# Kernel optimization log

Measured on AMD Instinct MI355X. Metric: run time of the kernel, lower is better.

## Reference

```python
import jax, jax.numpy as jnp
import numpy as np

E = 200_000   # edges (messages)
T = 2_000_000 # triplets
N = 20_000    # atoms/nodes
H = 128       # hidden_channels
INT = 64      # int_emb_size
BAS = 8       # basis_emb_size
OUT_EMB = 256 # out_emb_channels
NRAD = 6
SBF_DIM = 7 * 6  # num_spherical * num_radial = 42
NB = 4        # num_blocks
OUTC = 1      # num_targets


def setup_inputs() -> dict:
    key = jax.random.key(0)
    ks = iter(jax.random.split(key, 64))

    def w(shape):
        # glorot-ish scaled weights, stored as [in, out] for x @ W
        return jax.random.normal(next(ks), shape, jnp.float32) / np.sqrt(shape[-2])

    return dict(
        x=jax.random.normal(next(ks), (E, H), jnp.float32),
        rbf=jax.random.normal(next(ks), (E, NRAD), jnp.float32),
        sbf=jax.random.normal(next(ks), (T, SBF_DIM), jnp.float32),
        # interaction block params, stacked over NB blocks
        W_rbf1=w((NB, NRAD, BAS)), W_rbf2=w((NB, BAS, H)),
        W_sbf1=w((NB, SBF_DIM, BAS)), W_sbf2=w((NB, BAS, INT)),
        W_kj=w((NB, H, H)), b_kj=jnp.zeros((NB, H), jnp.float32),
        W_ji=w((NB, H, H)), b_ji=jnp.zeros((NB, H), jnp.float32),
        W_down=w((NB, H, INT)), W_up=w((NB, INT, H)),
        Wb=w((NB, 2, H, H)), bb=jnp.zeros((NB, 2, H), jnp.float32),   # num_before_skip=1 -> 2 linears
        Wa=w((NB, 4, H, H)), ba=jnp.zeros((NB, 4, H), jnp.float32),   # num_after_skip=2 -> 4 linears
        W_lin=w((NB, H, H)), b_lin=jnp.zeros((NB, H), jnp.float32),
        # output block params, stacked over NB+1 blocks
        Wo_rbf=w((NB + 1, NRAD, H)),
        Wo_up=w((NB + 1, H, OUT_EMB)), bo_up=jnp.zeros((NB + 1, OUT_EMB), jnp.float32),
        Wo_lins=w((NB + 1, 3, OUT_EMB, OUT_EMB)), bo_lins=jnp.zeros((NB + 1, 3, OUT_EMB), jnp.float32),
        Wo_out=w((NB + 1, OUT_EMB, OUTC)),
        idx_kj=jax.random.randint(next(ks), (T,), 0, E, jnp.int32),
        idx_ji=jax.random.randint(next(ks), (T,), 0, E, jnp.int32),
        idx_i=jax.random.randint(next(ks), (E,), 0, N, jnp.int32),
        num_nodes=N,
    )


def _interaction(b, x, rbf, sbf, idx_kj, idx_ji, p):
    act = jax.nn.silu
    x_ji = act(x @ p['W_ji'][b] + p['b_ji'][b])
    x_kj = act(x @ p['W_kj'][b] + p['b_kj'][b])
    rbf_t = (rbf @ p['W_rbf1'][b]) @ p['W_rbf2'][b]          # [E,H]
    x_kj = act((x_kj * rbf_t) @ p['W_down'][b])              # [E,INT]
    sbf_t = (sbf @ p['W_sbf1'][b]) @ p['W_sbf2'][b]          # [T,INT]
    m = x_kj[idx_kj] * sbf_t                                  # triplet gather [T,INT]
    agg = jax.ops.segment_sum(m, idx_ji, num_segments=x.shape[0])  # scatter-add [E,INT]
    x_kj = act(agg @ p['W_up'][b])                            # [E,H]
    h = x_ji + x_kj
    # residual layers before skip (1 layer = 2 linears)
    h = h + act(act(h @ p['Wb'][b, 0] + p['bb'][b, 0]) @ p['Wb'][b, 1] + p['bb'][b, 1])
    h = act(h @ p['W_lin'][b] + p['b_lin'][b]) + x
    # residual layers after skip (2 layers = 4 linears)
    for l in range(2):
        h = h + act(act(h @ p['Wa'][b, 2 * l] + p['ba'][b, 2 * l]) @ p['Wa'][b, 2 * l + 1] + p['ba'][b, 2 * l + 1])
    return h


def _output(b, x, rbf, idx_i, num_nodes, p):
    act = jax.nn.silu
    t = (rbf @ p['Wo_rbf'][b]) * x                            # [E,H]
    t = jax.ops.segment_sum(t, idx_i, num_segments=num_nodes) # [N,H]
    t = t @ p['Wo_up'][b] + p['bo_up'][b]
    for l in range(3):
        t = act(t @ p['Wo_lins'][b, l] + p['bo_lins'][b, l])
    return t @ p['Wo_out'][b]                                 # [N,OUTC]


def reference(x, rbf, sbf, W_rbf1, W_rbf2, W_sbf1, W_sbf2, W_kj, b_kj, W_ji, b_ji,
              W_down, W_up, Wb, bb, Wa, ba, W_lin, b_lin,
              Wo_rbf, Wo_up, bo_up, Wo_lins, bo_lins, Wo_out,
              idx_kj, idx_ji, idx_i, num_nodes):
    p = dict(W_rbf1=W_rbf1, W_rbf2=W_rbf2, W_sbf1=W_sbf1, W_sbf2=W_sbf2,
             W_kj=W_kj, b_kj=b_kj, W_ji=W_ji, b_ji=b_ji, W_down=W_down, W_up=W_up,
             Wb=Wb, bb=bb, Wa=Wa, ba=ba, W_lin=W_lin, b_lin=b_lin,
             Wo_rbf=Wo_rbf, Wo_up=Wo_up, bo_up=bo_up,
             Wo_lins=Wo_lins, bo_lins=bo_lins, Wo_out=Wo_out)
    P = _output(0, x, rbf, idx_i, num_nodes, p)
    for b in range(NB):  # fixed small layer loop
        x = _interaction(b, x, rbf, sbf, idx_kj, idx_ji, p)
        P = P + _output(b + 1, x, rbf, idx_i, num_nodes, p)
    return P
```

## Files before the change

kernel.cpp:

```cpp
#include <hip/hip_runtime.h>
#include <hip/hip_bf16.h>

#define E_EDGES 200000
#define T_TRIP  2000000
#define N_NODES 20000
#define H_DIM   128
#define INT_DIM 64
#define BAS     8
#define OUT_EMB 256
#define NRAD    6
#define SBF_D   42
#define NB      4

typedef __attribute__((ext_vector_type(8))) __bf16 bf16x8;
typedef __attribute__((ext_vector_type(4))) float f32x4;
typedef unsigned short u16;

__device__ __forceinline__ float silu_f(float v) { return v / (1.0f + __expf(-v)); }

__device__ __forceinline__ u16 f2bf(float f) {
    unsigned int u = __float_as_uint(f);
    u += 0x7FFF + ((u >> 16) & 1);
    return (u16)(u >> 16);
}
// ... 11 lines not shown
    int off = (row * stride + col0 * 2) ^ ((row & 7) << 4);
    *reinterpret_cast<ushort4*>(H + off) = hh;
    *reinterpret_cast<ushort4*>(L + off) = ll;
}
__device__ __forceinline__ void ld_split4(const char* H, const char* L, int row, int col0,
                                          int stride, float v[4]) {
    int off = (row * stride + col0 * 2) ^ ((row & 7) << 4);
    ushort4 hh = *reinterpret_cast<const ushort4*>(H + off);
    ushort4 ll = *reinterpret_cast<const ushort4*>(L + off);
    v[0] = bf2f(hh.x) + bf2f(ll.x);
    v[1] = bf2f(hh.y) + bf2f(ll.y);
    v[2] = bf2f(hh.z) + bf2f(ll.z);
    v[3] = bf2f(hh.w) + bf2f(ll.w);
}
__device__ __forceinline__ void st_bf4(char* T, int row, int col0, int stride,
                                       const float v[4]) {
    ushort4 hh;
    hh.x = f2bf(v[0]); hh.y = f2bf(v[1]); hh.z = f2bf(v[2]); hh.w = f2bf(v[3]);
    int off = (row * stride + col0 * 2) ^ ((row & 7) << 4);
    *reinterpret_cast<ushort4*>(T + off) = hh;
}

struct BF8x4 { bf16x8 h[4]; bf16x8 l[4]; };

__device__ __forceinline__ BF8x4 loadB128f(const u16* __restrict__ Bh, const u16* __restrict__ Bl,
                                           int k0, int wn, int l15, int khalf)
{
    BF8x4 f;
    #pragma unroll
    for (int n = 0; n < 4; ++n) {
        size_t bo = (size_t)(wn * 64 + n * 16 + l15) * 128 + k0 + khalf;
        f.h[n] = *reinterpret_cast<const bf16x8*>(Bh + bo);
        f.l[n] = *reinterpret_cast<const bf16x8*>(Bl + bo);
    }
    return f;
}
__device__ __forceinline__ BF8x4 loadB64f(const u16* __restrict__ Bh, const u16* __restrict__ Bl,
                                          int k0, int wn, int l15, int khalf)
{
    BF8x4 f;
    #pragma unroll
    for (int n = 0; n < 4; ++n) {
        size_t bo = (size_t)(wn * 64 + n * 16 + l15) * 64 + k0 + khalf;
        f.h[n] = *reinterpret_cast<const bf16x8*>(Bh + bo);
        f.l[n] = *reinterpret_cast<const bf16x8*>(Bl + bo);
    }
    return f;
}
__device__ __forceinline__ BF8x4 loadB256f(const u16* __restrict__ Bh, const u16* __restrict__ Bl,
                                           int k0, int wn, int l15, int khalf)
{
    BF8x4 f;
    #pragma unroll
    for (int n = 0; n < 4; ++n) {
        size_t bo = (size_t)(wn * 64 + n * 16 + l15) * 256 + k0 + khalf;
        f.h[n] = *reinterpret_cast<const bf16x8*>(Bh + bo);
        f.l[n] = *reinterpret_cast<const bf16x8*>(Bl + bo);
    }
    return f;
}

__device__ __forceinline__ void mfma_cluster(
    const char* AH, const char* AL, int k0, int wm, int l15, int khalf,
    const BF8x4& b, f32x4 acc[2][4])
{
    __builtin_amdgcn_s_setprio(1);
    #pragma unroll
    for (int m = 0; m < 2; ++m) {
        int row = wm * 32 + m * 16 + l15;
        int off = (row * 256 + (k0 + khalf) * 2) ^ ((row & 7) << 4);
        bf16x8 ah = *reinterpret_cast<const bf16x8*>(AH + off);
        bf16x8 al = *reinterpret_cast<const bf16x8*>(AL + off);
        #pragma unroll
        for (int n = 0; n < 4; ++n) {
            acc[m][n] = __builtin_amdgcn_mfma_f32_16x16x32_bf16(b.h[n], ah, acc[m][n], 0, 0, 0);
            acc[m][n] = __builtin_amdgcn_mfma_f32_16x16x32_bf16(b.h[n], al, acc[m][n], 0, 0, 0);
            acc[m][n] = __builtin_amdgcn_mfma_f32_16x16x32_bf16(b.l[n], ah, acc[m][n], 0, 0, 0);
        }
    }
    __builtin_amdgcn_s_setprio(0);
}
__device__ __forceinline__ void mfma_cluster_T(
    const char* T, int k0, int wm, int l15, int khalf,
    const BF8x4& b, f32x4 acc[2][4])
{
    __builtin_amdgcn_s_setprio(1);
    #pragma unroll
    for (int m = 0; m < 2; ++m) {
        int row = wm * 32 + m * 16 + l15;
        int off = (row * 256 + (k0 + khalf) * 2) ^ ((row & 7) << 4);
        bf16x8 a = *reinterpret_cast<const bf16x8*>(T + off);
        #pragma unroll
        for (int n = 0; n < 4; ++n) {
            acc[m][n] = __builtin_amdgcn_mfma_f32_16x16x32_bf16(b.h[n], a, acc[m][n], 0, 0, 0);
            acc[m][n] = __builtin_amdgcn_mfma_f32_16x16x32_bf16(b.l[n], a, acc[m][n], 0, 0, 0);
        }
    }
    __builtin_amdgcn_s_setprio(0);
}
__device__ __forceinline__ void mfma_cluster64_T(
    const char* T, int k0, int wm, int l15, int khalf,
    const BF8x4& b, f32x4 acc[2][4])
{
    __builtin_amdgcn_s_setprio(1);
    #pragma unroll
    for (int m = 0; m < 2; ++m) {
        int row = wm * 32 + m * 16 + l15;
        int off = (row * 128 + (k0 + khalf) * 2) ^ ((row & 7) << 4);
        bf16x8 a = *reinterpret_cast<const bf16x8*>(T + off);
        #pragma unroll
        for (int n = 0; n < 4; ++n) {
            acc[m][n] = __builtin_amdgcn_mfma_f32_16x16x32_bf16(b.h[n], a, acc[m][n], 0, 0, 0);
            acc[m][n] = __builtin_amdgcn_mfma_f32_16x16x32_bf16(b.l[n], a, acc[m][n], 0, 0, 0);
        }
    }
    __builtin_amdgcn_s_setprio(0);
}
__device__ __forceinline__ void mfma_cluster512(
    const char* AH, const char* AL, int k0, int l15, int khalf,
    const BF8x4& b, f32x4 acc[2][4])
{
    __builtin_amdgcn_s_setprio(1);
    #pragma unroll
    for (int m = 0; m < 2; ++m) {
        int row = m * 16 + l15;
        int off = (row * 512 + (k0 + khalf) * 2) ^ ((row & 7) << 4);
        bf16x8 ah = *reinterpret_cast<const bf16x8*>(AH + off);
        bf16x8 al = *reinterpret_cast<const bf16x8*>(AL + off);
        #pragma unroll
        for (int n = 0; n < 4; ++n) {
            acc[m][n] = __builtin_amdgcn_mfma_f32_16x16x32_bf16(b.h[n], ah, acc[m][n], 0, 0, 0);
            acc[m][n] = __builtin_amdgcn_mfma_f32_16x16x32_bf16(b.h[n], al, acc[m][n], 0, 0, 0);
            acc[m][n] = __builtin_amdgcn_mfma_f32_16x16x32_bf16(b.l[n], ah, acc[m][n], 0, 0, 0);
        }
    }
    __builtin_amdgcn_s_setprio(0);
}
__device__ __forceinline__ void mfma_cluster512_T(
    const char* T, int k0, int l15, int khalf,
    const BF8x4& b, f32x4 acc[2][4])
{
    __builtin_amdgcn_s_setprio(1);
    #pragma unroll
    for (int m = 0; m < 2; ++m) {
        int row = m * 16 + l15;
        int off = (row * 512 + (k0 + khalf) * 2) ^ ((row & 7) << 4);
        bf16x8 a = *reinterpret_cast<const bf16x8*>(T + off);
        #pragma unroll
        for (int n = 0; n < 4; ++n) {
            acc[m][n] = __builtin_amdgcn_mfma_f32_16x16x32_bf16(b.h[n], a, acc[m][n], 0, 0, 0);
            acc[m][n] = __builtin_amdgcn_mfma_f32_16x16x32_bf16(b.l[n], a, acc[m][n], 0, 0, 0);
        }
    }
    __builtin_amdgcn_s_setprio(0);
}

__device__ __forceinline__ void mm128_pipe(
    const char* AH, const char* AL,
    const u16* __restrict__ Bh, const u16* __restrict__ Bl, BF8x4& pre,
    const u16* __restrict__ nBh, const u16* __restrict__ nBl,
    int wm, int wn, int l15, int khalf, f32x4 acc[2][4])
{
    BF8x4 c0 = pre;
    BF8x4 c1 = loadB128f(Bh, Bl, 32, wn, l15, khalf);
    mfma_cluster(AH, AL, 0, wm, l15, khalf, c0, acc);
    BF8x4 c2 = loadB128f(Bh, Bl, 64, wn, l15, khalf);
    mfma_cluster(AH, AL, 32, wm, l15, khalf, c1, acc);
    BF8x4 c3 = loadB128f(Bh, Bl, 96, wn, l15, khalf);
    mfma_cluster(AH, AL, 64, wm, l15, khalf, c2, acc);
    if (nBh) pre = loadB128f(nBh, nBl, 0, wn, l15, khalf);
    mfma_cluster(AH, AL, 96, wm, l15, khalf, c3, acc);
}
__device__ __forceinline__ void mm128_pipe_T(
    const char* T,
    const u16* __restrict__ Bh, const u16* __restrict__ Bl, BF8x4& pre,
    const u16* __restrict__ nBh, const u16* __restrict__ nBl,
    int wm, int wn, int l15, int khalf, f32x4 acc[2][4])
{
    BF8x4 c0 = pre;
    BF8x4 c1 = loadB128f(Bh, Bl, 32, wn, l15, khalf);
    mfma_cluster_T(T, 0, wm, l15, khalf, c0, acc);
    BF8x4 c2 = loadB128f(Bh, Bl, 64, wn, l15, khalf);
    mfma_cluster_T(T, 32, wm, l15, khalf, c1, acc);
    BF8x4 c3 = loadB128f(Bh, Bl, 96, wn, l15, khalf);
    mfma_cluster_T(T, 64, wm, l15, khalf, c2, acc);
    if (nBh) pre = loadB128f(nBh, nBl, 0, wn, l15, khalf);
    mfma_cluster_T(T, 96, wm, l15, khalf, c3, acc);
}
__device__ __forceinline__ void mm64_pipe_T(
    const char* T,
    const u16* __restrict__ Bh, const u16* __restrict__ Bl, BF8x4& pre,
    const u16* __restrict__ nBh, const u16* __restrict__ nBl,
    int wm, int wn, int l15, int khalf, f32x4 acc[2][4])
{
    BF8x4 c0 = pre;
    BF8x4 c1 = loadB64f(Bh, Bl, 32, wn, l15, khalf);
    mfma_cluster64_T(T, 0, wm, l15, khalf, c0, acc);
    if (nBh) pre = loadB128f(nBh, nBl, 0, wn, l15, khalf);
    mfma_cluster64_T(T, 32, wm, l15, khalf, c1, acc);
}

__global__ __launch_bounds__(256) void wprep(
    const float* __restrict__ src, u16* __restrict__ hi,
    u16* __restrict__ lo, int K, int N)
{
    int e = blockIdx.x * 256 + threadIdx.x;
    int total = K * N;
    if (e >= total) return;
    size_t base = (size_t)blockIdx.y * total;
    float a = src[base + e];
    int k = e / N, n = e - k * N;
    u16 h = f2bf(a);
    u16 l = f2bf(a - bf2f(h));
    hi[base + (size_t)n * K + k] = h;
    lo[base + (size_t)n * K + k] = l;
}

__global__ __launch_bounds__(256) void cvt_bf(
    const float* __restrict__ src, u16* __restrict__ dst, int n4)
{
    int i = blockIdx.x * 256 + threadIdx.x;
    if (i >= n4) return;
    float4 f = *reinterpret_cast<const float4*>(&src[(size_t)i * 4]);
    ushort4 o;
    o.x = f2bf(f.x); o.y = f2bf(f.y); o.z = f2bf(f.z); o.w = f2bf(f.w);
    *reinterpret_cast<ushort4*>(&dst[(size_t)i * 4]) = o;
}

__global__ __launch_bounds__(256, 2) void pre_fuse(
    const u16* __restrict__ X, const float* __restrict__ rbf,
    const float* __restrict__ W1,
    const u16* __restrict__ Wjih, const u16* __restrict__ Wjil, const float* __restrict__ bji,
    const u16* __restrict__ Wkjh, const u16* __restrict__ Wkjl, const float* __restrict__ bkj,
    const float* __restrict__ Wr2,
    const u16* __restrict__ Wdnh, const u16* __restrict__ Wdnl,
    u16* __restrict__ E1, u16* __restrict__ C1)
{
    __shared__ char smem[32768];
    char* XT = smem;
    char* IT = smem + 16384;

    const int tid  = threadIdx.x;
    const int lane = tid & 63;
    const int w    = tid >> 6;
    const int wm   = w >> 1, wn = w & 1;
    const int bm   = blockIdx.x * 64;
    const int l15  = lane & 15;
    const int khalf = (lane >> 4) * 8;
    const int r4   = (lane >> 4) * 4;

    BF8x4 pre = loadB128f(Wjih, Wjil, 0, wn, l15, khalf);

    {
        int r  = tid >> 2;
        int c0 = (tid & 3) * 32;
        const u16* p = &X[(size_t)(bm + r) * H_DIM + c0];
        const int swz = (r & 7) << 4;
        #pragma unroll
        for (int q = 0; q < 4; ++q) {
            uint4 v = *reinterpret_cast<const uint4*>(p + q * 8);
            int off = (r * 256 + c0 * 2 + q * 16) ^ swz;
            *reinterpret_cast<uint4*>(XT + off) = v;
        }
    }
    __syncthreads();

    {
        f32x4 acc[2][4] = {};
        mm128_pipe_T(XT, Wjih, Wjil, pre, Wkjh, Wkjl, wm, wn, l15, khalf, acc);
        #pragma unroll
        for (int n = 0; n < 4; ++n) {
            int col0 = wn * 64 + n * 16 + r4;
            float4 bv = *reinterpret_cast<const float4*>(&bji[col0]);
            #pragma unroll
            for (int m = 0; m < 2; ++m) {
                int row = wm * 32 + m * 16 + l15;
                ushort4 ob;
                ob.x = f2bf(silu_f(acc[m][n][0] + bv.x));
                ob.y = f2bf(silu_f(acc[m][n][1] + bv.y));
                ob.z = f2bf(silu_f(acc[m][n][2] + bv.z));
                ob.w = f2bf(silu_f(acc[m][n][3] + bv.w));
                *reinterpret_cast<ushort4*>(&E1[(size_t)(bm + row) * H_DIM + col0]) = ob;
            }
        }
    }
    {
        f32x4 acc[2][4] = {};
        mm128_pipe_T(XT, Wkjh, Wkjl, pre, nullptr, nullptr, wm, wn, l15, khalf, acc);
        float r8v[2][8];
        #pragma unroll
        for (int m = 0; m < 2; ++m) {
            int grow = bm + wm * 32 + m * 16 + l15;
            const float2* rp = reinterpret_cast<const float2*>(&rbf[(size_t)grow * NRAD]);
            float2 q0 = rp[0], q1 = rp[1], q2 = rp[2];
            float rv[NRAD] = {q0.x, q0.y, q1.x, q1.y, q2.x, q2.y};
            #pragma unroll
            for (int j = 0; j < 8; ++j) r8v[m][j] = 0.f;
            #pragma unroll
            for (int k = 0; k < NRAD; ++k)
                #pragma unroll
                for (int j = 0; j < 8; ++j)
                    r8v[m][j] = fmaf(rv[k], W1[k * BAS + j], r8v[m][j]);
        }
        __syncthreads();
        #pragma unroll
        for (int n = 0; n < 4; ++n) {
            int col0 = wn * 64 + n * 16 + r4;
            float4 bvf = *reinterpret_cast<const float4*>(&bkj[col0]);
            float bv[4] = {bvf.x, bvf.y, bvf.z, bvf.w};
            float wrv[8][4];
            #pragma unroll
            for (int j = 0; j < 8; ++j) {
                float4 wf = *reinterpret_cast<const float4*>(&Wr2[j * H_DIM + col0]);
                wrv[j][0] = wf.x; wrv[j][1] = wf.y; wrv[j][2] = wf.z; wrv[j][3] = wf.w;
            }
            #pragma unroll
            for (int m = 0; m < 2; ++m) {
                int row = wm * 32 + m * 16 + l15;
                float v[4];
                #pragma unroll
                for (int r = 0; r < 4; ++r) {
                    float t = silu_f(acc[m][n][r] + bv[r]);
                    float g = 0.f;
                    #pragma unroll
                    for (int j = 0; j < 8; ++j)
                        g = fmaf(r8v[m][j], wrv[j][r], g);
                    v[r] = t * g;
                }
                st_bf4(IT, row, col0, 256, v);
            }
        }
    }
    __syncthreads();

    {
        f32x4 acc[2][2] = {};
        #pragma unroll
        for (int k0 = 0; k0 < 128; k0 += 32) {
            bf16x8 bh[2], bl[2];
            #pragma unroll
            for (int n = 0; n < 2; ++n) {
                size_t bo = (size_t)(wn * 32 + n * 16 + l15) * 128 + k0 + khalf;
                bh[n] = *reinterpret_cast<const bf16x8*>(Wdnh + bo);
                bl[n] = *reinterpret_cast<const bf16x8*>(Wdnl + bo);
            }
            __builtin_amdgcn_s_setprio(1);
            #pragma unroll
            for (int m = 0; m < 2; ++m) {
                int row = wm * 32 + m * 16 + l15;
                int off = (row * 256 + (k0 + khalf) * 2) ^ ((row & 7) << 4);
                bf16x8 a = *reinterpret_cast<const bf16x8*>(IT + off);
                #pragma unroll
                for (int n = 0; n < 2; ++n) {
                    acc[m][n] = __builtin_amdgcn_mfma_f32_16x16x32_bf16(bh[n], a, acc[m][n], 0, 0, 0);
                    acc[m][n] = __builtin_amdgcn_mfma_f32_16x16x32_bf16(bl[n], a, acc[m][n], 0, 0, 0);
                }
            }
            __builtin_amdgcn_s_setprio(0);
        }
        #pragma unroll
        for (int n = 0; n < 2; ++n) {
            int col0 = wn * 32 + n * 16 + r4;
            #pragma unroll
            for (int m = 0; m < 2; ++m) {
                int row = wm * 32 + m * 16 + l15;
                ushort4 ob;
                ob.x = f2bf(silu_f(acc[m][n][0]));
                ob.y = f2bf(silu_f(acc[m][n][1]));
                ob.z = f2bf(silu_f(acc[m][n][2]));
                ob.w = f2bf(silu_f(acc[m][n][3]));
                *reinterpret_cast<ushort4*>(&C1[(size_t)(bm + row) * INT_DIM + col0]) = ob;
            }
        }
    }
}

struct ChainP {
    const u16 *uph, *upl;
    const u16 *b0h, *b0l, *b1h, *b1l;
    const u16 *lnh, *lnl;
    const u16 *a0h, *a0l, *a1h, *a1l, *a2h, *a2l, *a3h, *a3l;
    const float *bb0, *bb1, *blin, *ba0, *ba1, *ba2, *ba3;
};
struct OutP {
    const float* TN;
    const u16 *Uh, *Ul; const float* bu;
    const u16 *L0h, *L0l; const float* b0;
    const u16 *L1h, *L1l; const float* b1;
    const u16 *L2h, *L2l; const float* b2;
    const float* Wo; float* P;
};

__device__ __forceinline__ void post_chain_body(
    char* smem, int bx,
    const u16* __restrict__ AGG, const u16* __restrict__ E1,
    const u16* __restrict__ X, const ChainP& p, u16* __restrict__ OUT)
{
    char* SH  = smem;
    char* SL  = smem + 16384;
    char* TMP = smem + 32768;
    char* GB  = TMP;

    const int tid  = threadIdx.x;
    const int lane = tid & 63;
    const int w    = tid >> 6;
    const int wm   = w >> 1, wn = w & 1;
    const int bm   = bx * 64;
    const int l15  = lane & 15;
    const int khalf = (lane >> 4) * 8;
    const int r4   = (lane >> 4) * 4;

    BF8x4 pre = loadB64f(p.uph, p.upl, 0, wn, l15, khalf);

    {
        int r  = tid >> 2;
        int c0 = (tid & 3) * 16;
        const ushort4* pg = reinterpret_cast<const ushort4*>(&AGG[(size_t)(bm + r) * INT_DIM + c0]);
        const int swz = (r & 7) << 4;
        #pragma unroll
        for (int q = 0; q < 4; ++q) {
            ushort4 v = pg[q];
            int off = (r * 128 + c0 * 2 + q * 8) ^ swz;
            *reinterpret_cast<ushort4*>(GB + off) = v;
        }
    }
    __syncthreads();

    f32x4 acc[2][4];
    #define ZACC { _Pragma("unroll") for (int m = 0; m < 2; ++m) \
                   _Pragma("unroll") for (int n = 0; n < 4; ++n) \
                       acc[m][n] = f32x4{0.f, 0.f, 0.f, 0.f}; }

    ZACC
    mm64_pipe_T(GB, p.uph, p.upl, pre, p.b0h, p.b0l, wm, wn, l15, khalf, acc);
    #pragma unroll
    for (int n = 0; n < 4; ++n) {
        int col0 = wn * 64 + n * 16 + r4;
        #pragma unroll
        for (int m = 0; m < 2; ++m) {
            int row = wm * 32 + m * 16 + l15;
            ushort4 e = *reinterpret_cast<const ushort4*>(&E1[(size_t)(bm + row) * H_DIM + col0]);
            float v[4];
            v[0] = bf2f(e.x) + silu_f(acc[m][n][0]);
            v[1] = bf2f(e.y) + silu_f(acc[m][n][1]);
            v[2] = bf2f(e.z) + silu_f(acc[m][n][2]);
            v[3] = bf2f(e.w) + silu_f(acc[m][n][3]);
            st_split4(SH, SL, row, col0, 256, v);
        }
    }
    __syncthreads();

    #define STAGE_PLAIN(WH, WL, BIAS, NWH, NWL)                                         \
    {                                                                                   \
        ZACC                                                                            \
        mm128_pipe(SH, SL, WH, WL, pre, NWH, NWL, wm, wn, l15, khalf, acc);             \
        _Pragma("unroll")                                                               \
        for (int n = 0; n < 4; ++n) {                                                   \
            int col0 = wn * 64 + n * 16 + r4;                                           \
            float4 bv = *reinterpret_cast<const float4*>(&BIAS[col0]);                  \
            _Pragma("unroll")                                                           \
            for (int m = 0; m < 2; ++m) {                                               \
                int row = wm * 32 + m * 16 + l15;                                       \
                float v[4];                                                             \
                v[0] = silu_f(acc[m][n][0] + bv.x);                                     \
                v[1] = silu_f(acc[m][n][1] + bv.y);                                     \
                v[2] = silu_f(acc[m][n][2] + bv.z);                                     \
                v[3] = silu_f(acc[m][n][3] + bv.w);                                     \
                st_bf4(TMP, row, col0, 256, v);                                         \
            }                                                                           \
        }                                                                               \
        __syncthreads();                                                                \
    }

    #define STAGE_RES(WH, WL, BIAS, NWH, NWL)                                           \
    {                                                                                   \
        ZACC                                                                            \
        mm128_pipe_T(TMP, WH, WL, pre, NWH, NWL, wm, wn, l15, khalf, acc);              \
        _Pragma("unroll")                                                               \
        for (int n = 0; n < 4; ++n) {                                                   \
            int col0 = wn * 64 + n * 16 + r4;                                           \
            float4 bv = *reinterpret_cast<const float4*>(&BIAS[col0]);                  \
            _Pragma("unroll")                                                           \
            for (int m = 0; m < 2; ++m) {                                               \
                int row = wm * 32 + m * 16 + l15;                                       \
                float v[4];                                                             \
                ld_split4(SH, SL, row, col0, 256, v);                                   \
                v[0] += silu_f(acc[m][n][0] + bv.x);                                    \
                v[1] += silu_f(acc[m][n][1] + bv.y);                                    \
                v[2] += silu_f(acc[m][n][2] + bv.z);                                    \
                v[3] += silu_f(acc[m][n][3] + bv.w);                                    \
                st_split4(SH, SL, row, col0, 256, v);                                   \
            }                                                                           \
        }                                                                               \
        __syncthreads();                                                                \
    }

    STAGE_PLAIN(p.b0h, p.b0l, p.bb0, p.b1h, p.b1l)
    STAGE_RES(p.b1h, p.b1l, p.bb1, p.lnh, p.lnl)

    {
        ZACC
        mm128_pipe(SH, SL, p.lnh, p.lnl, pre, p.a0h, p.a0l, wm, wn, l15, khalf, acc);
        __syncthreads();
        #pragma unroll
        for (int n = 0; n < 4; ++n) {
            int col0 = wn * 64 + n * 16 + r4;
            float4 bv = *reinterpret_cast<const float4*>(&p.blin[col0]);
            #pragma unroll
            for (int m = 0; m < 2; ++m) {
                int row = wm * 32 + m * 16 + l15;
                ushort4 xv = *reinterpret_cast<const ushort4*>(&X[(size_t)(bm + row) * H_DIM + col0]);
                float v[4];
                v[0] = silu_f(acc[m][n][0] + bv.x) + bf2f(xv.x);
                v[1] = silu_f(acc[m][n][1] + bv.y) + bf2f(xv.y);
                v[2] = silu_f(acc[m][n][2] + bv.z) + bf2f(xv.z);
                v[3] = silu_f(acc[m][n][3] + bv.w) + bf2f(xv.w);
                st_split4(SH, SL, row, col0, 256, v);
            }
        }
        __syncthreads();
    }

    STAGE_PLAIN(p.a0h, p.a0l, p.ba0, p.a1h, p.a1l)
    STAGE_RES(p.a1h, p.a1l, p.ba1, p.a2h, p.a2l)
    STAGE_PLAIN(p.a2h, p.a2l, p.ba2, p.a3h, p.a3l)

    {
        ZACC
        mm128_pipe_T(TMP, p.a3h, p.a3l, pre, nullptr, nullptr, wm, wn, l15, khalf, acc);
        #pragma unroll
        for (int n = 0; n < 4; ++n) {
            int col0 = wn * 64 + n * 16 + r4;
            float4 bv = *reinterpret_cast<const float4*>(&p.ba3[col0]);
            #pragma unroll
            for (int m = 0; m < 2; ++m) {
                int row = wm * 32 + m * 16 + l15;
                float v[4];
                ld_split4(SH, SL, row, col0, 256, v);
                ushort4 ob;
                ob.x = f2bf(v[0] + silu_f(acc[m][n][0] + bv.x));
                ob.y = f2bf(v[1] + silu_f(acc[m][n][1] + bv.y));
                ob.z = f2bf(v[2] + silu_f(acc[m][n][2] + bv.z));
                ob.w = f2bf(v[3] + silu_f(acc[m][n][3] + bv.w));
                *reinterpret_cast<ushort4*>(&OUT[(size_t)(bm + row) * H_DIM + col0]) = ob;
            }
        }
    }
    #undef STAGE_PLAIN
    #undef STAGE_RES
    #undef ZACC
}

__device__ __forceinline__ void out_chain_body(char* smem, int bx, const OutP& o)
{
    char* SH  = smem;
    char* SL  = smem + 16384;
    char* TMP = smem + 32768;
    char* XH  = TMP;
    char* XL  = TMP + 8192;

    const int tid  = threadIdx.x;
    const int lane = tid & 63;
    const int wn   = tid >> 6;
    const int bm   = bx * 32;
    const int l15  = lane & 15;
    const int khalf = (lane >> 4) * 8;
    const int r4   = (lane >> 4) * 4;

    {
        int r  = tid >> 3;
        int c0 = (tid & 7) * 16;
        const float* p = &o.TN[(size_t)(bm + r) * H_DIM + c0];
        const int swz = (r & 7) << 4;
        #pragma unroll
        for (int q = 0; q < 4; ++q) {
            float4 f = *reinterpret_cast<const float4*>(p + q * 4);
            float vv[4] = {f.x, f.y, f.z, f.w};
            u16 h[4], l[4];
            #pragma unroll
            for (int j = 0; j < 4; ++j) {
                h[j] = f2bf(vv[j]);
                l[j] = f2bf(vv[j] - bf2f(h[j]));
            }
            int off = (r * 256 + c0 * 2 + q * 8) ^ swz;
            *reinterpret_cast<ushort4*>(XH + off) = make_ushort4(h[0], h[1], h[2], h[3]);
            *reinterpret_cast<ushort4*>(XL + off) = make_ushort4(l[0], l[1], l[2], l[3]);
        }
    }
    __syncthreads();

    f32x4 acc[2][4];
    #define ZACC { _Pragma("unroll") for (int m = 0; m < 2; ++m) \
                   _Pragma("unroll") for (int n = 0; n < 4; ++n) \
                       acc[m][n] = f32x4{0.f, 0.f, 0.f, 0.f}; }

    {
        ZACC
        BF8x4 cur = loadB128f(o.Uh, o.Ul, 0, wn, l15, khalf);
        #pragma unroll
        for (int k = 0; k < 4; ++k) {
            BF8x4 nxt;
            if (k < 3) nxt = loadB128f(o.Uh, o.Ul, 32 * (k + 1), wn, l15, khalf);
            mfma_cluster(XH, XL, 32 * k, 0, l15, khalf, cur, acc);
            if (k < 3) cur = nxt;
        }
        __syncthreads();
        #pragma unroll
        for (int n = 0; n < 4; ++n) {
            int col0 = wn * 64 + n * 16 + r4;
            float4 bv = *reinterpret_cast<const float4*>(&o.bu[col0]);
            #pragma unroll
            for (int m = 0; m < 2; ++m) {
                int row = m * 16 + l15;
                float v[4] = {acc[m][n][0] + bv.x, acc[m][n][1] + bv.y,
                              acc[m][n][2] + bv.z, acc[m][n][3] + bv.w};
                st_split4(SH, SL, row, col0, 512, v);
            }
        }
        __syncthreads();
    }

    {
        ZACC
        BF8x4 cur = loadB256f(o.L0h, o.L0l, 0, wn, l15, khalf);
        #pragma unroll
        for (int k = 0; k < 8; ++k) {
            BF8x4 nxt;
            if (k < 7) nxt = loadB256f(o.L0h, o.L0l, 32 * (k + 1), wn, l15, khalf);
            mfma_cluster512(SH, SL, 32 * k, l15, khalf, cur, acc);
            if (k < 7) cur = nxt;
        }
        #pragma unroll
        for (int n = 0; n < 4; ++n) {
            int col0 = wn * 64 + n * 16 + r4;
            float4 bv = *reinterpret_cast<const float4*>(&o.b0[col0]);
            #pragma unroll
            for (int m = 0; m < 2; ++m) {
                int row = m * 16 + l15;
                float v[4];
                v[0] = silu_f(acc[m][n][0] + bv.x);
                v[1] = silu_f(acc[m][n][1] + bv.y);
                v[2] = silu_f(acc[m][n][2] + bv.z);
                v[3] = silu_f(acc[m][n][3] + bv.w);
                st_bf4(TMP, row, col0, 512, v);
            }
        }
        __syncthreads();
    }

    {
        ZACC
        BF8x4 cur = loadB256f(o.L1h, o.L1l, 0, wn, l15, khalf);
        #pragma unroll
        for (int k = 0; k < 8; ++k) {
            BF8x4 nxt;
            if (k < 7) nxt = loadB256f(o.L1h, o.L1l, 32 * (k + 1), wn, l15, khalf);
            mfma_cluster512_T(TMP, 32 * k, l15, khalf, cur, acc);
            if (k < 7) cur = nxt;
        }
        #pragma unroll
        for (int n = 0; n < 4; ++n) {
            int col0 = wn * 64 + n * 16 + r4;
            float4 bv = *reinterpret_cast<const float4*>(&o.b1[col0]);
            #pragma unroll
            for (int m = 0; m < 2; ++m) {
                int row = m * 16 + l15;
                float v[4];
                v[0] = silu_f(acc[m][n][0] + bv.x);
                v[1] = silu_f(acc[m][n][1] + bv.y);
                v[2] = silu_f(acc[m][n][2] + bv.z);
                v[3] = silu_f(acc[m][n][3] + bv.w);
                st_split4(SH, SL, row, col0, 512, v);
            }
        }
        __syncthreads();
    }

    {
        ZACC
        BF8x4 cur = loadB256f(o.L2h, o.L2l, 0, wn, l15, khalf);
        #pragma unroll
        for (int k = 0; k < 8; ++k) {
            BF8x4 nxt;
            if (k < 7) nxt = loadB256f(o.L2h, o.L2l, 32 * (k + 1), wn, l15, khalf);
            mfma_cluster512(SH, SL, 32 * k, l15, khalf, cur, acc);
            if (k < 7) cur = nxt;
        }
        __syncthreads();
        #pragma unroll
        for (int n = 0; n < 4; ++n) {
            int col0 = wn * 64 + n * 16 + r4;
            float4 bv = *reinterpret_cast<const float4*>(&o.b2[col0]);
            #pragma unroll
            for (int m = 0; m < 2; ++m) {
                int row = m * 16 + l15;
                float v[4];
                v[0] = silu_f(acc[m][n][0] + bv.x);
                v[1] = silu_f(acc[m][n][1] + bv.y);
                v[2] = silu_f(acc[m][n][2] + bv.z);
                v[3] = silu_f(acc[m][n][3] + bv.w);
                st_split4(SH, SL, row, col0, 512, v);
            }
        }
        __syncthreads();
    }

    {
        int row  = tid >> 3;
        int part = tid & 7;
        float s = 0.f;
        int cbase = part * 32;
        #pragma unroll
        for (int c4 = 0; c4 < 32; c4 += 4) {
            float v[4];
            ld_split4(SH, SL, row, cbase + c4, 512, v);
            float4 wv = *reinterpret_cast<const float4*>(&o.Wo[cbase + c4]);
            s = fmaf(v[0], wv.x, s);
            s = fmaf(v[1], wv.y, s);
            s = fmaf(v[2], wv.z, s);
            s = fmaf(v[3], wv.w, s);
        }
        s += __shfl_xor(s, 1);
        s += __shfl_xor(s, 2);
        s += __shfl_xor(s, 4);
        if (part == 0) o.P[bm + row] += s;
    }
    #undef ZACC
}

__global__ __launch_bounds__(256, 2) void post_fused(
    int npost,
    const u16* __restrict__ AGG, const u16* __restrict__ E1,
    const u16* __restrict__ X, ChainP p, u16* __restrict__ OUT, OutP o)
{
    __shared__ char smem[49152];
    if ((int)blockIdx.x < npost)
        post_chain_body(smem, blockIdx.x, AGG, E1, X, p, OUT);
    else
        out_chain_body(smem, blockIdx.x - npost, o);
}

__device__ __forceinline__ float dot8_bf(uint4 r, const float* w2) {
    float s;
    s  = bf2f((u16)(r.x)) * w2[0] + bf2f((u16)(r.x >> 16)) * w2[1];
    s += bf2f((u16)(r.y)) * w2[2] + bf2f((u16)(r.y >> 16)) * w2[3];
    s += bf2f((u16)(r.z)) * w2[4] + bf2f((u16)(r.z >> 16)) * w2[5];
    s += bf2f((u16)(r.w)) * w2[6] + bf2f((u16)(r.w >> 16)) * w2[7];
    return s;
}

__device__ __forceinline__ void triplet_body(
    int bx, int nblk,
    const u16* __restrict__ ps8b, const float* __restrict__ Wsb2,
    const u16* __restrict__ xkj, const int* __restrict__ pkj,
    const int* __restrict__ tptr, const int* __restrict__ tcnt,
    u16* __restrict__ agg)
{
    const int lane = threadIdx.x & 63;
    int wid = bx * 4 + (threadIdx.x >> 6);
    const int nw = nblk * 4;
    float w2[BAS];
    #pragma unroll
    for (int j = 0; j < BAS; ++j) w2[j] = Wsb2[j * INT_DIM + lane];

    for (int e = wid; e < E_EDGES; e += nw) {
        int start = tptr[e];
        int end   = start + tcnt[e];
        float acc0 = 0.f, acc1 = 0.f;
        int i = start;
        for (; i + 1 < end; i += 2) {
            uint4 ra = *reinterpret_cast<const uint4*>(&ps8b[(size_t)i * BAS]);
            uint4 rb = *reinterpret_cast<const uint4*>(&ps8b[(size_t)(i + 1) * BAS]);
            int e0 = pkj[i], e1 = pkj[i + 1];
            float s0 = dot8_bf(ra, w2);
            float s1 = dot8_bf(rb, w2);
            acc0 = fmaf(bf2f(xkj[(size_t)e0 * INT_DIM + lane]), s0, acc0);
            acc1 = fmaf(bf2f(xkj[(size_t)e1 * INT_DIM + lane]), s1, acc1);
        }
        if (i < end) {
            uint4 ra = *reinterpret_cast<const uint4*>(&ps8b[(size_t)i * BAS]);
            int e0 = pkj[i];
            acc0 = fmaf(bf2f(xkj[(size_t)e0 * INT_DIM + lane]), dot8_bf(ra, w2), acc0);
        }
        agg[(size_t)e * INT_DIM + lane] = f2bf(acc0 + acc1);
    }
}

__device__ __forceinline__ void out_gather_body(
    int bx, int nblk,
    const float* __restrict__ rbf, const float* __restrict__ Wor,
    const u16* __restrict__ x,
    const int* __restrict__ eptr, const int* __restrict__ ecnt,
    const int* __restrict__ eperm, float* __restrict__ tN)
{
    const int lane = threadIdx.x & 63;
    int wid = bx * 4 + (threadIdx.x >> 6);
    const int nw = nblk * 4;
    float wr0[NRAD], wr1[NRAD];
    #pragma unroll
    for (int k = 0; k < NRAD; ++k) {
        wr0[k] = Wor[k * H_DIM + lane];
        wr1[k] = Wor[k * H_DIM + lane + 64];
    }
    for (int n = wid; n < N_NODES; n += nw) {
        int start = eptr[n];
        int end   = start + ecnt[n];
        float a0 = 0.f, a1 = 0.f;
        for (int i = start; i < end; ++i) {
            int e = eperm[i];
            const float2* rp = reinterpret_cast<const float2*>(&rbf[(size_t)e * NRAD]);
            float2 r0 = rp[0], r1 = rp[1], r2 = rp[2];
            float rA = r0.x*wr0[0] + r0.y*wr0[1] + r1.x*wr0[2]
                     + r1.y*wr0[3] + r2.x*wr0[4] + r2.y*wr0[5];
            float rB = r0.x*wr1[0] + r0.y*wr1[1] + r1.x*wr1[2]
                     + r1.y*wr1[3] + r2.x*wr1[4] + r2.y*wr1[5];
            a0 = fmaf(rA, bf2f(x[(size_t)e * H_DIM + lane]), a0);
            a1 = fmaf(rB, bf2f(x[(size_t)e * H_DIM + lane + 64]), a1);
        }
        tN[(size_t)n * H_DIM + lane] = a0;
        tN[(size_t)n * H_DIM + lane + 64] = a1;
    }
}

__global__ __launch_bounds__(256) void gather_fused(
    int GT,
    const u16* __restrict__ ps8b, const float* __restrict__ Wsb2,
    const u16* __restrict__ xkj, const int* __restrict__ pkj,
    const int* __restrict__ tptr, const int* __restrict__ tcnt,
    u16* __restrict__ agg,
    const float* __restrict__ rbf, const float* __restrict__ Wor,
    const u16* __restrict__ x,
    const int* __restrict__ eptr, const int* __restrict__ ecnt,
    const int* __restrict__ eperm, float* __restrict__ tN)
{
    int bx = blockIdx.x;
    if (bx < GT)
        triplet_body(bx, GT, ps8b, Wsb2, xkj, pkj, tptr, tcnt, agg);
    else
        out_gather_body(bx - GT, gridDim.x - GT, rbf, Wor, x, eptr, ecnt, eperm, tN);
}

__global__ __launch_bounds__(256) void csr_count(
    const int* __restrict__ idx, int* __restrict__ cnt, int n)
{
    int i = blockIdx.x * 256 + threadIdx.x;
    if (i < n) atomicAdd(&cnt[idx[i]], 1);
}

__global__ __launch_bounds__(256) void scan_block(
    const int* __restrict__ cnt, int* __restrict__ ptr, int* __restrict__ bsum, int n)
{
    __shared__ int s[256];
    int i = blockIdx.x * 256 + threadIdx.x;
    int v = (i < n) ? cnt[i] : 0;
    s[threadIdx.x] = v;
    __syncthreads();
    #pragma unroll
    for (int off = 1; off < 256; off <<= 1) {
        int t = (threadIdx.x >= off) ? s[threadIdx.x - off] : 0;
        __syncthreads();
        s[threadIdx.x] += t;
        __syncthreads();
    }
    if (i < n) ptr[i] = s[threadIdx.x] - v;
    if (threadIdx.x == 255) bsum[blockIdx.x] = s[255];
}

__global__ __launch_bounds__(1024) void scan_aux(int* __restrict__ bsum, int nb)
{
    __shared__ int s[1024];
    int v = (threadIdx.x < nb) ? bsum[threadIdx.x] : 0;
    s[threadIdx.x] = v;
    __syncthreads();
    #pragma unroll
    for (int off = 1; off < 1024; off <<= 1) {
        int t = (threadIdx.x >= off) ? s[threadIdx.x - off] : 0;
        __syncthreads();
        s[threadIdx.x] += t;
        __syncthreads();
    }
    if (threadIdx.x < nb) bsum[threadIdx.x] = s[threadIdx.x] - v;
}

__global__ __launch_bounds__(256) void scan_add(
    int* __restrict__ ptr, const int* __restrict__ bsum, int n)
{
    int i = blockIdx.x * 256 + threadIdx.x;
    if (i < n) ptr[i] += bsum[blockIdx.x];
}

__global__ __launch_bounds__(256) void csr_fill(
    const int* __restrict__ idx, int* __restrict__ cursor,
    int* __restrict__ perm, int n)
{
    int i = blockIdx.x * 256 + threadIdx.x;
    if (i >= n) return;
    int pos = atomicAdd(&cursor[idx[i]], 1);
    perm[pos] = i;
}

__global__ __launch_bounds__(256) void permute_s8(
    const float* __restrict__ sbf, const float* __restrict__ W1all,
    const int* __restrict__ idx_kj, const int* __restrict__ tperm,
    u16* __restrict__ ps8, int* __restrict__ pkj, int Tcount)
{
    __shared__ float Ws[NB * SBF_D * BAS];
    for (int i = threadIdx.x; i < NB * SBF_D * BAS; i += 256) Ws[i] = W1all[i];
    __syncthreads();
    int i = blockIdx.x * 256 + threadIdx.x;
    if (i >= Tcount) return;
    int t = tperm[i];
    pkj[i] = idx_kj[t];
    float s[SBF_D];
    {
        const float2* p2 = reinterpret_cast<const float2*>(&sbf[(size_t)t * SBF_D]);
        #pragma unroll
        for (int k = 0; k < SBF_D / 2; ++k) {
            float2 v = p2[k];
            s[2 * k] = v.x; s[2 * k + 1] = v.y;
        }
    }
    #pragma unroll
    for (int b = 0; b < NB; ++b) {
        const float* Wb_ = &Ws[b * SBF_D * BAS];
        float acc[BAS] = {};
        for (int k = 0; k < SBF_D; ++k) {
            float sv = s[k];
            #pragma unroll
            for (int j = 0; j < BAS; ++j)
                acc[j] = fmaf(sv, Wb_[k * BAS + j], acc[j]);
        }
        ushort4 o0 = make_ushort4(f2bf(acc[0]), f2bf(acc[1]), f2bf(acc[2]), f2bf(acc[3]));
        ushort4 o1 = make_ushort4(f2bf(acc[4]), f2bf(acc[5]), f2bf(acc[6]), f2bf(acc[7]));
        u16* op = &ps8[((size_t)b * Tcount + i) * BAS];
        *reinterpret_cast<ushort4*>(op) = o0;
        *reinterpret_cast<ushort4*>(op + 4) = o1;
    }
}

extern "C" void kernel_launch(void* const* d_in, const int* in_sizes, int n_in,
                              void* d_out, int out_size, void* d_ws, size_t ws_size,
                              hipStream_t stream)
{
    const float* x_in    = (const float*)d_in[0];
    const float* rbf     = (const float*)d_in[1];
    const float* sbf     = (const float*)d_in[2];
    const float* W_rbf1  = (const float*)d_in[3];
    const float* W_rbf2  = (const float*)d_in[4];
    const float* W_sbf1  = (const float*)d_in[5];
    const float* W_sbf2  = (const float*)d_in[6];
    const float* W_kj    = (const float*)d_in[7];
    const float* b_kj    = (const float*)d_in[8];
    const float* W_ji    = (const float*)d_in[9];
    const float* b_ji    = (const float*)d_in[10];
    const float* W_down  = (const float*)d_in[11];
    const float* W_up    = (const float*)d_in[12];
    const float* Wb      = (const float*)d_in[13];
    const float* bb      = (const float*)d_in[14];
    const float* Wa      = (const float*)d_in[15];
    const float* ba      = (const float*)d_in[16];
    const float* W_lin   = (const float*)d_in[17];
    const float* b_lin   = (const float*)d_in[18];
    const float* Wo_rbf  = (const float*)d_in[19];
    const float* Wo_up   = (const float*)d_in[20];
    const float* bo_up   = (const float*)d_in[21];
    const float* Wo_lins = (const float*)d_in[22];
    const float* bo_lins = (const float*)d_in[23];
    const float* Wo_out  = (const float*)d_in[24];
    const int*   idx_kj  = (const int*)d_in[25];
    const int*   idx_ji  = (const int*)d_in[26];
    const int*   idx_i   = (const int*)d_in[27];

    char* ws = (char*)d_ws;
    size_t off = 0;
    auto alloc = [&](size_t bytes) -> void* {
        void* p = (void*)(ws + off);
        off += (bytes + 255) & ~(size_t)255;
        return p;
    };
    u16*   X0B = (u16*)alloc((size_t)E_EDGES * H_DIM * 2);
    u16*   XAB = (u16*)alloc((size_t)E_EDGES * H_DIM * 2);
    u16*   XBB = (u16*)alloc((size_t)E_EDGES * H_DIM * 2);
    u16*   E1B = (u16*)alloc((size_t)E_EDGES * H_DIM * 2);
    u16*   C1B = (u16*)alloc((size_t)E_EDGES * INT_DIM * 2);
    u16*   C2B = (u16*)alloc((size_t)E_EDGES * INT_DIM * 2);
    float* TN  = (float*)alloc((size_t)N_NODES * H_DIM * 4);
    u16* HKJ = (u16*)alloc(4  * 16384 * 2); u16* LKJ = (u16*)alloc(4  * 16384 * 2);
    u16* HJI = (u16*)alloc(4  * 16384 * 2); u16* LJI = (u16*)alloc(4  * 16384 * 2);
    u16* HDN = (u16*)alloc(4  * 8192  * 2); u16* LDN = (u16*)alloc(4  * 8192  * 2);
    u16* HUP = (u16*)alloc(4  * 8192  * 2); u16* LUP = (u16*)alloc(4  * 8192  * 2);
    u16* HWB = (u16*)alloc(8  * 16384 * 2); u16* LWB = (u16*)alloc(8  * 16384 * 2);
    u16* HWA = (u16*)alloc(16 * 16384 * 2); u16* LWA = (u16*)alloc(16 * 16384 * 2);
    u16* HLN = (u16*)alloc(4  * 16384 * 2); u16* LLN = (u16*)alloc(4  * 16384 * 2);
    u16* HOU = (u16*)alloc(5  * 32768 * 2); u16* LOU = (u16*)alloc(5  * 32768 * 2);
    u16* HOL = (u16*)alloc(15 * 65536 * 2); u16* LOL = (u16*)alloc(15 * 65536 * 2);
    int* tcnt  = (int*)alloc((size_t)E_EDGES * 4);
    int* tptr  = (int*)alloc((size_t)E_EDGES * 4);
    int* tcur  = (int*)alloc((size_t)E_EDGES * 4);
    int* tperm = (int*)alloc((size_t)T_TRIP * 4);
    int* tbsum = (int*)alloc(1024 * 4);
    int* ecnt  = (int*)alloc((size_t)N_NODES * 4);
    int* eptr  = (int*)alloc((size_t)N_NODES * 4);
    int* ecur  = (int*)alloc((size_t)N_NODES * 4);
    int* eperm = (int*)alloc((size_t)E_EDGES * 4);
    int* ebsum = (int*)alloc(1024 * 4);
    u16* PS8 = (u16*)alloc((size_t)NB * T_TRIP * BAS * 2);
    int* PKJ = (int*)alloc((size_t)T_TRIP * 4);
    (void)ws_size;

    auto prep = [&](const float* src, u16* hi, u16* lo, int K, int N, int cnt) {
        dim3 g((K * N + 255) / 256, cnt);
        hipLaunchKernelGGL(wprep, g, dim3(256), 0, stream, src, hi, lo, K, N);
    };
    prep(W_kj,    HKJ, LKJ, 128, 128, 4);
    prep(W_ji,    HJI, LJI, 128, 128, 4);
    prep(W_down,  HDN, LDN, 128, 64,  4);
    prep(W_up,    HUP, LUP, 64,  128, 4);
    prep(Wb,      HWB, LWB, 128, 128, 8);
    prep(Wa,      HWA, LWA, 128, 128, 16);
    prep(W_lin,   HLN, LLN, 128, 128, 4);
    prep(Wo_up,   HOU, LOU, 128, 256, 5);
    prep(Wo_lins, HOL, LOL, 256, 256, 15);

    hipLaunchKernelGGL(cvt_bf, dim3((E_EDGES * H_DIM / 4 + 255) / 256), dim3(256), 0, stream,
                       x_in, X0B, E_EDGES * H_DIM / 4);

    {
        const int nbT = (E_EDGES + 255) / 256;
        hipMemsetAsync(tcnt, 0, (size_t)E_EDGES * 4, stream);
        hipLaunchKernelGGL(csr_count, dim3((T_TRIP + 255) / 256), dim3(256), 0, stream,
                           idx_ji, tcnt, T_TRIP);
        hipLaunchKernelGGL(scan_block, dim3(nbT), dim3(256), 0, stream, tcnt, tptr, tbsum, E_EDGES);
        hipLaunchKernelGGL(scan_aux, dim3(1), dim3(1024), 0, stream, tbsum, nbT);
        hipLaunchKernelGGL(scan_add, dim3(nbT), dim3(256), 0, stream, tptr, tbsum, E_EDGES);
        hipMemcpyAsync(tcur, tptr, (size_t)E_EDGES * 4, hipMemcpyDeviceToDevice, stream);
        hipLaunchKernelGGL(csr_fill, dim3((T_TRIP + 255) / 256), dim3(256), 0, stream,
                           idx_ji, tcur, tperm, T_TRIP);
    }
    {
        const int nbN = (N_NODES + 255) / 256;
        hipMemsetAsync(ecnt, 0, (size_t)N_NODES * 4, stream);
        hipLaunchKernelGGL(csr_count, dim3((E_EDGES + 255) / 256), dim3(256), 0, stream,
                           idx_i, ecnt, E_EDGES);
        hipLaunchKernelGGL(scan_block, dim3(nbN), dim3(256), 0, stream, ecnt, eptr, ebsum, N_NODES);
        hipLaunchKernelGGL(scan_aux, dim3(1), dim3(1024), 0, stream, ebsum, nbN);
        hipLaunchKernelGGL(scan_add, dim3(nbN), dim3(256), 0, stream, eptr, ebsum, N_NODES);
        hipMemcpyAsync(ecur, eptr, (size_t)N_NODES * 4, hipMemcpyDeviceToDevice, stream);
        hipLaunchKernelGGL(csr_fill, dim3((E_EDGES + 255) / 256), dim3(256), 0, stream,
                           idx_i, ecur, eperm, E_EDGES);
    }
    hipLaunchKernelGGL(permute_s8, dim3((T_TRIP + 255) / 256), dim3(256), 0, stream,
                       sbf, W_sbf1, idx_kj, tperm, PS8, PKJ, T_TRIP);

    float* P = (float*)d_out;
    hipMemsetAsync(P, 0, (size_t)N_NODES * sizeof(float), stream);

    auto make_outp = [&](int ob) {
        OutP o;
        o.TN = TN;
        o.Uh = HOU + (size_t)ob * 32768; o.Ul = LOU + (size_t)ob * 32768;
        o.bu = bo_up + (size_t)ob * OUT_EMB;
        o.L0h = HOL + (size_t)(ob * 3 + 0) * 65536; o.L0l = LOL + (size_t)(ob * 3 + 0) * 65536;
        o.b0 = bo_lins + (size_t)(ob * 3 + 0) * OUT_EMB;
        o.L1h = HOL + (size_t)(ob * 3 + 1) * 65536; o.L1l = LOL + (size_t)(ob * 3 + 1) * 65536;
        o.b1 = bo_lins + (size_t)(ob * 3 + 1) * OUT_EMB;
        o.L2h = HOL + (size_t)(ob * 3 + 2) * 65536; o.L2l = LOL + (size_t)(ob * 3 + 2) * 65536;
        o.b2 = bo_lins + (size_t)(ob * 3 + 2) * OUT_EMB;
        o.Wo = Wo_out + (size_t)ob * OUT_EMB;
        o.P = P;
        return o;
    };

    const u16* xcur = X0B;
    const int EB = E_EDGES / 64;
    const int GT = 2048;
    for (int b = 0; b < NB; ++b) {
        u16* xnext = (b % 2 == 0) ? XAB : XBB;
        hipLaunchKernelGGL(pre_fuse, dim3(EB), dim3(256), 0, stream,
                           xcur, rbf, W_rbf1 + (size_t)b * NRAD * BAS,
                           HJI + (size_t)b * 16384, LJI + (size_t)b * 16384, b_ji + (size_t)b * H_DIM,
                           HKJ + (size_t)b * 16384, LKJ + (size_t)b * 16384, b_kj + (size_t)b * H_DIM,
                           W_rbf2 + (size_t)b * BAS * H_DIM,
                           HDN + (size_t)b * 8192, LDN + (size_t)b * 8192,
                           E1B, C1B);
        hipLaunchKernelGGL(gather_fused, dim3(GT + 2048), dim3(256), 0, stream,
                           GT,
                           PS8 + (size_t)b * T_TRIP * BAS, W_sbf2 + (size_t)b * BAS * INT_DIM,
                           C1B, PKJ, tptr, tcnt, C2B,
                           rbf, Wo_rbf + (size_t)b * NRAD * H_DIM, xcur,
                           eptr, ecnt, eperm, TN);
        ChainP cp;
        cp.uph = HUP + (size_t)b * 8192;  cp.upl = LUP + (size_t)b * 8192;
        cp.b0h = HWB + (size_t)(b * 2 + 0) * 16384; cp.b0l = LWB + (size_t)(b * 2 + 0) * 16384;
        cp.b1h = HWB + (size_t)(b * 2 + 1) * 16384; cp.b1l = LWB + (size_t)(b * 2 + 1) * 16384;
        cp.lnh = HLN + (size_t)b * 16384; cp.lnl = LLN + (size_t)b * 16384;
        cp.a0h = HWA + (size_t)(b * 4 + 0) * 16384; cp.a0l = LWA + (size_t)(b * 4 + 0) * 16384;
        cp.a1h = HWA + (size_t)(b * 4 + 1) * 16384; cp.a1l = LWA + (size_t)(b * 4 + 1) * 16384;
        cp.a2h = HWA + (size_t)(b * 4 + 2) * 16384; cp.a2l = LWA + (size_t)(b * 4 + 2) * 16384;
        cp.a3h = HWA + (size_t)(b * 4 + 3) * 16384; cp.a3l = LWA + (size_t)(b * 4 + 3) * 16384;
        cp.bb0 = bb + (size_t)(b * 2 + 0) * H_DIM;
        cp.bb1 = bb + (size_t)(b * 2 + 1) * H_DIM;
        cp.blin = b_lin + (size_t)b * H_DIM;
        cp.ba0 = ba + (size_t)(b * 4 + 0) * H_DIM;
        cp.ba1 = ba + (size_t)(b * 4 + 1) * H_DIM;
        cp.ba2 = ba + (size_t)(b * 4 + 2) * H_DIM;
        cp.ba3 = ba + (size_t)(b * 4 + 3) * H_DIM;
        OutP op = make_outp(b);
        hipLaunchKernelGGL(post_fused, dim3(EB + N_NODES / 32), dim3(256), 0, stream,
                           EB, C2B, E1B, xcur, cp, xnext, op);
        xcur = xnext;
    }
    {
        OutP op = make_outp(NB);
        ChainP cp = {};
        hipLaunchKernelGGL(gather_fused, dim3(2048), dim3(256), 0, stream,
                           0,
                           PS8, W_sbf2, C1B, PKJ, tptr, tcnt, C2B,
                           rbf, Wo_rbf + (size_t)NB * NRAD * H_DIM, xcur,
                           eptr, ecnt, eperm, TN);
        hipLaunchKernelGGL(post_fused, dim3(N_NODES / 32), dim3(256), 0, stream,
                           0, C2B, E1B, xcur, cp, XAB, op);
    }
}
```

Baseline: 3.890 ms.

## Fuse next block's pre-projection into post chain kernel tail

The per-block pre_fuse work for block b+1 (x_ji, x_kj with rbf gating, and the down projection) now runs at the end of post_fused for block b. It reuses the freshly computed output tile kept in shared memory, so the next block no longer re-reads x from global memory and one kernel launch per block goes away. A __syncthreads in pre_fuse is also removed. In exchange the post kernel carries more registers and code, which may lower its occupancy. Because E1B is read by the post chain and also written by the fused tail, correctness depends on each block reading only its own rows.

```diff
diff --git a/kernel.cpp b/kernel.cpp
--- a/kernel.cpp
+++ b/kernel.cpp
@@ -337,7 +337,6 @@
                 for (int j = 0; j < 8; ++j)
                     r8v[m][j] = fmaf(rv[k], W1[k * BAS + j], r8v[m][j]);
         }
-        __syncthreads();
         #pragma unroll
         for (int n = 0; n < 4; ++n) {
             int col0 = wn * 64 + n * 16 + r4;
@@ -416,6 +415,10 @@
     const u16 *lnh, *lnl;
     const u16 *a0h, *a0l, *a1h, *a1l, *a2h, *a2l, *a3h, *a3l;
     const float *bb0, *bb1, *blin, *ba0, *ba1, *ba2, *ba3;
+    int doPre;
+    const float *rbfp, *preW1, *nbji, *nbkj, *nwr2;
+    const u16 *njih, *njil, *nkjh, *nkjl, *ndnh, *ndnl;
+    u16 *nE1, *nC1;
 };
 struct OutP {
     const float* TN;
@@ -562,7 +565,9 @@
 
     {
         ZACC
-        mm128_pipe_T(TMP, p.a3h, p.a3l, pre, nullptr, nullptr, wm, wn, l15, khalf, acc);
+        mm128_pipe_T(TMP, p.a3h, p.a3l, pre,
+                     p.doPre ? p.njih : nullptr, p.doPre ? p.njil : nullptr,
+                     wm, wn, l15, khalf, acc);
         #pragma unroll
         for (int n = 0; n < 4; ++n) {
             int col0 = wn * 64 + n * 16 + r4;
@@ -578,6 +583,124 @@
                 ob.z = f2bf(v[2] + silu_f(acc[m][n][2] + bv.z));
                 ob.w = f2bf(v[3] + silu_f(acc[m][n][3] + bv.w));
                 *reinterpret_cast<ushort4*>(&OUT[(size_t)(bm + row) * H_DIM + col0]) = ob;
+                if (p.doPre) {
+                    int offx = (row * 256 + col0 * 2) ^ ((row & 7) << 4);
+                    *reinterpret_cast<ushort4*>(SH + offx) = ob;
+                }
+            }
+        }
+    }
+
+    if (p.doPre) {
+        char* XT = SH;
+        char* IT = SL;
+        __syncthreads();
+
+        {
+            ZACC
+            mm128_pipe_T(XT, p.njih, p.njil, pre, p.nkjh, p.nkjl, wm, wn, l15, khalf, acc);
+            #pragma unroll
+            for (int n = 0; n < 4; ++n) {
+                int col0 = wn * 64 + n * 16 + r4;
+                float4 bv = *reinterpret_cast<const float4*>(&p.nbji[col0]);
+                #pragma unroll
+                for (int m = 0; m < 2; ++m) {
+                    int row = wm * 32 + m * 16 + l15;
+                    ushort4 ob;
+                    ob.x = f2bf(silu_f(acc[m][n][0] + bv.x));
+                    ob.y = f2bf(silu_f(acc[m][n][1] + bv.y));
+                    ob.z = f2bf(silu_f(acc[m][n][2] + bv.z));
+                    ob.w = f2bf(silu_f(acc[m][n][3] + bv.w));
+                    *reinterpret_cast<ushort4*>(&p.nE1[(size_t)(bm + row) * H_DIM + col0]) = ob;
+                }
+            }
+        }
+        {
+            ZACC
+            mm128_pipe_T(XT, p.nkjh, p.nkjl, pre, nullptr, nullptr, wm, wn, l15, khalf, acc);
+            float r8v[2][8];
+            #pragma unroll
+            for (int m = 0; m < 2; ++m) {
+                int grow = bm + wm * 32 + m * 16 + l15;
+                const float2* rp = reinterpret_cast<const float2*>(&p.rbfp[(size_t)grow * NRAD]);
+                float2 q0 = rp[0], q1 = rp[1], q2 = rp[2];
+                float rv[NRAD] = {q0.x, q0.y, q1.x, q1.y, q2.x, q2.y};
+                #pragma unroll
+                for (int j = 0; j < 8; ++j) r8v[m][j] = 0.f;
+                #pragma unroll
+                for (int k = 0; k < NRAD; ++k)
+                    #pragma unroll
+                    for (int j = 0; j < 8; ++j)
+                        r8v[m][j] = fmaf(rv[k], p.preW1[k * BAS + j], r8v[m][j]);
+            }
+            #pragma unroll
+            for (int n = 0; n < 4; ++n) {
+                int col0 = wn * 64 + n * 16 + r4;
+                float4 bvf = *reinterpret_cast<const float4*>(&p.nbkj[col0]);
+                float bv[4] = {bvf.x, bvf.y, bvf.z, bvf.w};
+                float wrv[8][4];
+                #pragma unroll
+                for (int j = 0; j < 8; ++j) {
+                    float4 wf = *reinterpret_cast<const float4*>(&p.nwr2[j * H_DIM + col0]);
+                    wrv[j][0] = wf.x; wrv[j][1] = wf.y; wrv[j][2] = wf.z; wrv[j][3] = wf.w;
+                }
+                #pragma unroll
+                for (int m = 0; m < 2; ++m) {
+                    int row = wm * 32 + m * 16 + l15;
+                    float v[4];
+                    #pragma unroll
+                    for (int r = 0; r < 4; ++r) {
+                        float t = silu_f(acc[m][n][r] + bv[r]);
+                        float g = 0.f;
+                        #pragma unroll
+                        for (int j = 0; j < 8; ++j)
+                            g = fmaf(r8v[m][j], wrv[j][r], g);
+                        v[r] = t * g;
+                    }
+                    st_bf4(IT, row, col0, 256, v);
+                }
+            }
+        }
+        __syncthreads();
+
+        {
+            f32x4 acc2[2][2] = {};
+            #pragma unroll
+            for (int k0 = 0; k0 < 128; k0 += 32) {
+                bf16x8 bh[2], bl[2];
+                #pragma unroll
+                for (int n = 0; n < 2; ++n) {
+                    size_t bo = (size_t)(wn * 32 + n * 16 + l15) * 128 + k0 + khalf;
+                    bh[n] = *reinterpret_cast<const bf16x8*>(p.ndnh + bo);
+                    bl[n] = *reinterpret_cast<const bf16x8*>(p.ndnl + bo);
+                }
+                __builtin_amdgcn_s_setprio(1);
+                #pragma unroll
+                for (int m = 0; m < 2; ++m) {
+                    int row = wm * 32 + m * 16 + l15;
+                    int off = (row * 256 + (k0 + khalf) * 2) ^ ((row & 7) << 4);
+                    bf16x8 a = *reinterpret_cast<const bf16x8*>(IT + off);
+                    #pragma unroll
+                    for (int n = 0; n < 2; ++n) {
+                        acc2[m][n] = __builtin_amdgcn_mfma_f32_16x16x32_bf16(bh[n], a, acc2[m][n], 0, 0, 0);
+                        acc2[m][n] = __builtin_amdgcn_mfma_f32_16x16x32_bf16(bl[n], a, acc2[m][n], 0, 0, 0);
+                    }
+                }
+                __builtin_amdgcn_s_setprio(0);
+            }
+            #pragma unroll
+            for (int n = 0; n < 2; ++n) {
+                int col0 = wn * 32 + n * 16 + r4;
+                #pragma unroll
+                for (int m = 0; m < 2; ++m) {
+                    int row = wm * 32 + m * 16 + l15;
+                    ushort4 ob;
+                    ob.x = f2bf(silu_f(acc2[m][n][0]));
+                    ob.y = f2bf(silu_f(acc2[m][n][1]));
+                    ob.z = f2bf(silu_f(acc2[m][n][2]));
+                    ob.w = f2bf(silu_f(acc2[m][n][3]));
+                    *reinterpret_cast<ushort4*>(&p.nC1[(size_t)(bm + row) * INT_DIM + col0]) = ob;
+                }
             }
         }
     }
@@ -1109,15 +1232,17 @@
     const u16* xcur = X0B;
     const int EB = E_EDGES / 64;
     const int GT = 2048;
+
+    hipLaunchKernelGGL(pre_fuse, dim3(EB), dim3(256), 0, stream,
+                       xcur, rbf, W_rbf1,
+                       HJI, LJI, b_ji,
+                       HKJ, LKJ, b_kj,
+                       W_rbf2,
+                       HDN, LDN,
+                       E1B, C1B);
+
     for (int b = 0; b < NB; ++b) {
         u16* xnext = (b % 2 == 0) ? XAB : XBB;
-        hipLaunchKernelGGL(pre_fuse, dim3(EB), dim3(256), 0, stream,
-                           xcur, rbf, W_rbf1 + (size_t)b * NRAD * BAS,
-                           HJI + (size_t)b * 16384, LJI + (size_t)b * 16384, b_ji + (size_t)b * H_DIM,
-                           HKJ + (size_t)b * 16384, LKJ + (size_t)b * 16384, b_kj + (size_t)b * H_DIM,
-                           W_rbf2 + (size_t)b * BAS * H_DIM,
-                           HDN + (size_t)b * 8192, LDN + (size_t)b * 8192,
-                           E1B, C1B);
         hipLaunchKernelGGL(gather_fused, dim3(GT + 2048), dim3(256), 0, stream,
                            GT,
                            PS8 + (size_t)b * T_TRIP * BAS, W_sbf2 + (size_t)b * BAS * INT_DIM,
@@ -1140,6 +1265,26 @@
         cp.ba1 = ba + (size_t)(b * 4 + 1) * H_DIM;
         cp.ba2 = ba + (size_t)(b * 4 + 2) * H_DIM;
         cp.ba3 = ba + (size_t)(b * 4 + 3) * H_DIM;
+        if (b < NB - 1) {
+            int nb_ = b + 1;
+            cp.doPre = 1;
+            cp.rbfp  = rbf;
+            cp.preW1 = W_rbf1 + (size_t)nb_ * NRAD * BAS;
+            cp.njih = HJI + (size_t)nb_ * 16384; cp.njil = LJI + (size_t)nb_ * 16384;
+            cp.nbji = b_ji + (size_t)nb_ * H_DIM;
+            cp.nkjh = HKJ + (size_t)nb_ * 16384; cp.nkjl = LKJ + (size_t)nb_ * 16384;
+            cp.nbkj = b_kj + (size_t)nb_ * H_DIM;
+            cp.nwr2 = W_rbf2 + (size_t)nb_ * BAS * H_DIM;
+            cp.ndnh = HDN + (size_t)nb_ * 8192; cp.ndnl = LDN + (size_t)nb_ * 8192;
+            cp.nE1  = E1B; cp.nC1 = C1B;
+        } else {
+            cp.doPre = 0;
+            cp.rbfp = nullptr; cp.preW1 = nullptr;
+            cp.njih = nullptr; cp.njil = nullptr; cp.nbji = nullptr;
+            cp.nkjh = nullptr; cp.nkjl = nullptr; cp.nbkj = nullptr;
+            cp.nwr2 = nullptr; cp.ndnh = nullptr; cp.ndnl = nullptr;
+            cp.nE1 = nullptr; cp.nC1 = nullptr;
+        }
         OutP op = make_outp(b);
         hipLaunchKernelGGL(post_fused, dim3(EB + N_NODES / 32), dim3(256), 0, stream,
                            EB, C2B, E1B, xcur, cp, xnext, op);
```

After: 3.878 ms. About the same (-0.3%).
